# Performance work log

Measured on AMD Instinct MI355X. Metric: run time of the kernel, lower is better.

Reference implementation:

```python
import jax, jax.numpy as jnp
import numpy as np


def setup_inputs() -> dict:
    key = jax.random.key(0)
    k1, k2 = jax.random.split(key)
    B, N = 8192, 8192
    inputs = jax.random.normal(k1, (B, N), dtype=jnp.float32)
    targets = jax.random.randint(k2, (B,), 0, N, dtype=jnp.int64)
    return {"inputs": inputs, "targets": targets}


def reference(inputs, targets):
    # targ_bin[i, j] = 1 if j < targets[i] else 0  (broadcasted, no loop)
    N = inputs.shape[1]
    targ_bin = (jnp.arange(N)[None, :] < targets[:, None]).astype(inputs.dtype)
    # BCEWithLogitsLoss (mean): softplus(x) - x*t, numerically stable
    loss = jnp.mean(jax.nn.softplus(inputs) - inputs * targ_bin)
    return loss
```

## Files before the change

kernel.cpp:

```cpp
#include <hip/hip_runtime.h>


__global__ __launch_bounds__(256) void bce_reduce_kernel(
    const float4* __restrict__ in,
    const int*    __restrict__ tgt,
    float*        __restrict__ out,
    int nvec,
    int row_shift,
    int row_mask,
    float inv_count)
{
    float acc = 0.f;
    const int stride = gridDim.x * blockDim.x;
    for (int v = blockIdx.x * blockDim.x + threadIdx.x; v < nvec; v += stride) {
        float4 x = in[v];
        int row = v >> row_shift;
        int col = (v & row_mask) << 2;
        int t   = tgt[row];
        float s;
        s  = fmaxf(x.x, 0.f) + __logf(1.f + __expf(-fabsf(x.x))) - ((col + 0) < t ? x.x : 0.f);
        s += fmaxf(x.y, 0.f) + __logf(1.f + __expf(-fabsf(x.y))) - ((col + 1) < t ? x.y : 0.f);
        s += fmaxf(x.z, 0.f) + __logf(1.f + __expf(-fabsf(x.z))) - ((col + 2) < t ? x.z : 0.f);
        s += fmaxf(x.w, 0.f) + __logf(1.f + __expf(-fabsf(x.w))) - ((col + 3) < t ? x.w : 0.f);
        acc += s;
    }

    #pragma unroll
    for (int off = 32; off > 0; off >>= 1)
        acc += __shfl_down(acc, off, 64);

    __shared__ float wave_sums[4];
    const int lane = threadIdx.x & 63;
    const int wave = threadIdx.x >> 6;
    if (lane == 0) wave_sums[wave] = acc;
    __syncthreads();
    if (threadIdx.x == 0) {
        float b = wave_sums[0] + wave_sums[1] + wave_sums[2] + wave_sums[3];
        atomicAdd(out, b * inv_count);
    }
}

extern "C" void kernel_launch(void* const* d_in, const int* in_sizes, int n_in,
                              void* d_out, int out_size, void* d_ws, size_t ws_size,
                              hipStream_t stream) {
    const float* in  = (const float*)d_in[0];
    const int*   tgt = (const int*)d_in[1];
    float*       out = (float*)d_out;

    const long long total = (long long)in_sizes[0];
    const int B = in_sizes[1];
    const int N = (int)(total / B);
    const int nvec = (int)(total / 4);
    const int nvec_per_row = N / 4;
    const int row_shift = __builtin_ctz(nvec_per_row);
    const int row_mask  = nvec_per_row - 1;
    const float inv_count = 1.0f / (float)total;

    hipMemsetAsync(d_out, 0, sizeof(float), stream);

    const int block = 256;
    const int grid  = 2048;
    bce_reduce_kernel<<<grid, block, 0, stream>>>(
        (const float4*)in, tgt, out, nvec, row_shift, row_mask, inv_count);
}
```

Measured before the change: 353.4 us.

## Unroll contiguous block loads and rewrite softplus as separate abs/sign/log sums

Each block now processes a contiguous chunk with four independent float4 loads per iteration, instead of a grid-stride loop. Softplus minus x*t is rewritten as 0.5*(±x + |x|) + ln2*log2(1+2^(-|x|*log2e)), accumulated in three separate sums and using the raw exp2/log builtins. This aims to raise memory-level parallelism and cut per-element ALU work. The chunking assumes nvec divides evenly by grid*1024 and has no tail handling.

```diff
diff --git a/kernel.cpp b/kernel.cpp
--- a/kernel.cpp
+++ b/kernel.cpp
@@ -10,20 +10,55 @@
     int row_mask,
     float inv_count)
 {
-    float acc = 0.f;
-    const int stride = gridDim.x * blockDim.x;
-    for (int v = blockIdx.x * blockDim.x + threadIdx.x; v < nvec; v += stride) {
-        float4 x = in[v];
-        int row = v >> row_shift;
-        int col = (v & row_mask) << 2;
-        int t   = tgt[row];
-        float s;
-        s  = fmaxf(x.x, 0.f) + __logf(1.f + __expf(-fabsf(x.x))) - ((col + 0) < t ? x.x : 0.f);
-        s += fmaxf(x.y, 0.f) + __logf(1.f + __expf(-fabsf(x.y))) - ((col + 1) < t ? x.y : 0.f);
-        s += fmaxf(x.z, 0.f) + __logf(1.f + __expf(-fabsf(x.z))) - ((col + 2) < t ? x.z : 0.f);
-        s += fmaxf(x.w, 0.f) + __logf(1.f + __expf(-fabsf(x.w))) - ((col + 3) < t ? x.w : 0.f);
-        acc += s;
+    const float LOG2E = 1.44269504088896340736f;
+
+    float su = 0.f;
+    float sa = 0.f;
+    float sl = 0.f;
+
+    const int per_block = nvec / gridDim.x;
+    const int base = blockIdx.x * per_block;
+    const int iters = per_block / (4 * 256);
+
+    for (int it = 0; it < iters; ++it) {
+        int i0 = base + (it * 4 + 0) * 256 + threadIdx.x;
+        int i1 = base + (it * 4 + 1) * 256 + threadIdx.x;
+        int i2 = base + (it * 4 + 2) * 256 + threadIdx.x;
+        int i3 = base + (it * 4 + 3) * 256 + threadIdx.x;
+        float4 x0 = in[i0];
+        float4 x1 = in[i1];
+        float4 x2 = in[i2];
+        float4 x3 = in[i3];
+        int t0 = tgt[i0 >> row_shift];
+        int t1 = tgt[i1 >> row_shift];
+        int t2 = tgt[i2 >> row_shift];
+        int t3 = tgt[i3 >> row_shift];
+        int c0 = (i0 & row_mask) << 2;
+        int c1 = (i1 & row_mask) << 2;
+        int c2 = (i2 & row_mask) << 2;
+        int c3 = (i3 & row_mask) << 2;
+
+#define ELEM(xv, cc, tt)                                                      \
+        {                                                                     \
+            float xe = (xv);                                                  \
+            su += ((cc) < (tt)) ? -xe : xe;                                   \
+            sa += fabsf(xe);                                                  \
+            sl += __builtin_amdgcn_logf(                                      \
+                      1.f + __builtin_amdgcn_exp2f(-fabsf(xe) * LOG2E));      \
+        }
+
+        ELEM(x0.x, c0 + 0, t0) ELEM(x0.y, c0 + 1, t0)
+        ELEM(x0.z, c0 + 2, t0) ELEM(x0.w, c0 + 3, t0)
+        ELEM(x1.x, c1 + 0, t1) ELEM(x1.y, c1 + 1, t1)
+        ELEM(x1.z, c1 + 2, t1) ELEM(x1.w, c1 + 3, t1)
+        ELEM(x2.x, c2 + 0, t2) ELEM(x2.y, c2 + 1, t2)
+        ELEM(x2.z, c2 + 2, t2) ELEM(x2.w, c2 + 3, t2)
+        ELEM(x3.x, c3 + 0, t3) ELEM(x3.y, c3 + 1, t3)
+        ELEM(x3.z, c3 + 2, t3) ELEM(x3.w, c3 + 3, t3)
+#undef ELEM
     }
+
+    float acc = 0.5f * (su + sa) + 0.69314718055994530942f * sl;
 
     #pragma unroll
     for (int off = 32; off > 0; off >>= 1)
@@ -56,7 +91,7 @@
     const int row_mask  = nvec_per_row - 1;
     const float inv_count = 1.0f / (float)total;
 
-    hipMemsetAsync(d_out, 0, sizeof(float), stream);
+    (void)hipMemsetAsync(d_out, 0, sizeof(float), stream);
 
     const int block = 256;
     const int grid  = 2048;
```

Result: no change. 360.1 us (+1.9%).
